# Kernel optimization log

Hardware: AMD Instinct MI355X
Metric: run time of the kernel (lower is better)

Reference implementation:

```python
import jax, jax.numpy as jnp
import numpy as np

PF_DIM = 1024
F_DIM = 1024
LOW = 128
MID = 32  # low_dim // 4
BATCH = 8192


def setup_inputs() -> dict:
    key = jax.random.key(0)
    ks = jax.random.split(key, 10)
    s = lambda fan_in: 1.0 / np.sqrt(fan_in)
    return {
        "f": jax.random.normal(ks[0], (BATCH, F_DIM), jnp.float32),
        "pf": jax.random.normal(ks[1], (BATCH, PF_DIM), jnp.float32),
        # nn.Linear weights are (out, in)
        "proj_f_w": jax.random.uniform(ks[2], (LOW, F_DIM), jnp.float32, -s(F_DIM), s(F_DIM)),
        "proj_f_b": jax.random.uniform(ks[3], (LOW,), jnp.float32, -s(F_DIM), s(F_DIM)),
        "proj_pf_w": jax.random.uniform(ks[4], (LOW, PF_DIM), jnp.float32, -s(PF_DIM), s(PF_DIM)),
        "proj_pf_b": jax.random.uniform(ks[5], (LOW,), jnp.float32, -s(PF_DIM), s(PF_DIM)),
        "proj_f2_w": jax.random.uniform(ks[6], (F_DIM, LOW), jnp.float32, -s(LOW), s(LOW)),
        "proj_f2_b": jax.random.uniform(ks[7], (F_DIM,), jnp.float32, -s(LOW), s(LOW)),
        "pg_w": jax.random.uniform(ks[8], (2 * LOW * MID, LOW), jnp.float32, -s(LOW), s(LOW)),
        "pg_b": jax.random.uniform(ks[9], (2 * LOW * MID,), jnp.float32, -s(LOW), s(LOW)),
    }


def reference(f, pf, proj_f_w, proj_f_b, proj_pf_w, proj_pf_b,
              proj_f2_w, proj_f2_b, pg_w, pg_b):
    b = pf.shape[0]
    # project both inputs to low_dim
    f_low = f @ proj_f_w.T + proj_f_b              # (b, LOW)
    pf_low = pf @ proj_pf_w.T + proj_pf_b          # (b, LOW)
    # per-sample generated weights
    params = pf_low @ pg_w.T + pg_b                # (b, 2*LOW*MID)
    dim = LOW * MID
    p1 = params[:, :dim].reshape(b, LOW, MID)      # (b, LOW, MID)
    p2 = params[:, dim:].reshape(b, MID, LOW)      # (b, MID, LOW)
    # batched tiny MLP: (b,1,LOW)@(b,LOW,MID) -> relu -> @(b,MID,LOW)
    h = jax.nn.relu(jnp.einsum('bl,blm->bm', f_low, p1))
    g = jnp.einsum('bm,bml->bl', h, p2)            # (b, LOW)
    out = g @ proj_f2_w.T + proj_f2_b + f + pf     # (b, F_DIM)
    return out
```

## Files before the change

### kernel.cpp

```cpp
#include <hip/hip_runtime.h>
#include <hip/hip_bf16.h>
#include <stdint.h>


typedef __attribute__((ext_vector_type(8))) short bf16x8;
typedef __attribute__((ext_vector_type(4))) float f32x4;

#define MFMA(a, b, c) __builtin_amdgcn_mfma_f32_16x16x32_bf16((a), (b), (c), 0, 0, 0)

__device__ __forceinline__ ushort f2bf(float x) {
    union { float f; uint32_t u; } v; v.f = x;
    return (ushort)((v.u + 0x7FFFu + ((v.u >> 16) & 1u)) >> 16);
}
__device__ __forceinline__ ushort4 f2bf4(float4 v) {
    ushort4 o; o.x = f2bf(v.x); o.y = f2bf(v.y); o.z = f2bf(v.z); o.w = f2bf(v.w); return o;
}

__global__ __launch_bounds__(256) void k0_convert(
    const float* __restrict__ pgw, const float* __restrict__ wf,
    const float* __restrict__ wpf, const float* __restrict__ w2,
    ushort* __restrict__ pg_img, ushort* __restrict__ w_img, ushort* __restrict__ w2_img)
{
    int cid = blockIdx.x * 256 + threadIdx.x;
    const float* src; ushort* dst;
    if (cid < 131072) {
        int lane = cid & 63, ks = (cid >> 6) & 3, T = cid >> 8;
        int j = T * 16 + (lane & 15), k = ks * 32 + (lane >> 4) * 8;
        src = pgw + (size_t)j * 128 + k;
        dst = pg_img + (size_t)cid * 8;
    } else if (cid < 163840) {
        int c = cid - 131072;
        int lane = c & 63, ks = (c >> 6) & 31, lt = (c >> 11) & 7, mat = c >> 14;
        int l = lt * 16 + (lane & 15), k = ks * 32 + (lane >> 4) * 8;
        src = (mat ? wpf : wf) + (size_t)l * 1024 + k;
        dst = w_img + (size_t)c * 8;
    } else {
        int c = cid - 163840;
        int lane = c & 63, ks = (c >> 6) & 3, nt = c >> 8;
        int n = nt * 16 + (lane & 15), k = ks * 32 + (lane >> 4) * 8;
        src = w2 + (size_t)n * 128 + k;
        dst = w2_img + (size_t)c * 8;
    }
    float4 a = ((const float4*)src)[0], b = ((const float4*)src)[1];
    ((ushort4*)dst)[0] = f2bf4(a);
    ((ushort4*)dst)[1] = f2bf4(b);
}

__global__ __launch_bounds__(256, 4) void k1_proj(
    const float* __restrict__ f, const float* __restrict__ pf,
    const ushort* __restrict__ w_img,
    const float* __restrict__ bf_bias, const float* __restrict__ bpf_bias,
    float* __restrict__ f_low , ushort* __restrict__ pf_img )
{
    __shared__ __align__(16) ushort As[16 * 1032];
    __shared__ __align__(16) ushort Tr[16 * 136];
    const int tid = threadIdx.x;
    const int lane = tid & 63, wid = tid >> 6;
    const int q = lane >> 4, r15 = lane & 15;
    const int mat = blockIdx.x & 1;
    const int b0 = (blockIdx.x >> 1) * 16;
    const float* src = mat ? pf : f;
    const float* bias_ptr = mat ? bpf_bias : bf_bias;

#pragma unroll
    for (int ch = 0; ch < 2; ch++) {
        float4 v[8];
#pragma unroll
        for (int rr = 0; rr < 8; rr++)
            v[rr] = *(const float4*)(src + (size_t)(b0 + ch * 8 + rr) * 1024 + tid * 4);
#pragma unroll
        for (int rr = 0; rr < 8; rr++)
            *(ushort4*)(As + (ch * 8 + rr) * 1032 + tid * 4) = f2bf4(v[rr]);
    }
    float bias_v[2];
#pragma unroll
    for (int j = 0; j < 2; j++) bias_v[j] = bias_ptr[wid * 32 + j * 16 + r15];
    __syncthreads();

    const int lt0 = wid * 2;
    const ushort* wb = w_img + (size_t)mat * 131072;
    bf16x8 wfr[4][2];
#pragma unroll
    for (int pre = 0; pre < 4; pre++)
#pragma unroll
        for (int j = 0; j < 2; j++)
            wfr[pre][j] = *(const bf16x8*)(wb + ((size_t)(lt0 + j) * 32 + pre) * 512 + lane * 8);

    f32x4 c[2];
    c[0] = (f32x4){0.f, 0.f, 0.f, 0.f};
    c[1] = (f32x4){0.f, 0.f, 0.f, 0.f};
#pragma unroll
    for (int ks = 0; ks < 32; ks++) {
        const int cur = ks & 3;
        bf16x8 af = *(const bf16x8*)(As + r15 * 1032 + ks * 32 + q * 8);
        c[0] = MFMA(af, wfr[cur][0], c[0]);
        c[1] = MFMA(af, wfr[cur][1], c[1]);
        if (ks + 4 < 32) {
#pragma unroll
            for (int j = 0; j < 2; j++)
                wfr[cur][j] = *(const bf16x8*)(wb + ((size_t)(lt0 + j) * 32 + (ks + 4)) * 512 + lane * 8);
        }
    }
    if (mat == 0) {
#pragma unroll
        for (int j = 0; j < 2; j++) {
            int l = wid * 32 + j * 16 + r15;
#pragma unroll
            for (int r = 0; r < 4; r++)
                f_low[(size_t)l * 8192 + b0 + q * 4 + r] = c[j][r] + bias_v[j];
        }
    } else {
#pragma unroll
        for (int j = 0; j < 2; j++) {
            int l = wid * 32 + j * 16 + r15;
#pragma unroll
            for (int r = 0; r < 4; r++)
                Tr[(q * 4 + r) * 136 + l] = f2bf(c[j][r] + bias_v[j]);
        }
        __syncthreads();
        int ks2 = tid >> 6, ln = tid & 63;
        int b_loc = ln & 15, k0 = ks2 * 32 + (ln >> 4) * 8;
        uint4 tv = *(const uint4*)(Tr + b_loc * 136 + k0);
        *(uint4*)(pf_img + ((size_t)((b0 >> 4) * 4 + ks2)) * 512 + (size_t)ln * 8) = tv;
    }
}

__global__ __launch_bounds__(256, 4) void k2_h(
    const ushort* __restrict__ pg_img, const ushort* __restrict__ pf_img,
    const float* __restrict__ pg_b, const float* __restrict__ f_low,
    float* __restrict__ h_part )
{
    __shared__ __align__(16) float flow[16 * 32];
    __shared__ __align__(16) float biasl[512];
    __shared__ __align__(16) float hred[4 * 32 * 32];
    const int tid = threadIdx.x;
    const int lane = tid & 63, wid = tid >> 6;
    const int q = lane >> 4, r15 = lane & 15;
    const int jg = blockIdx.x & 7, sb = blockIdx.x >> 3;
    const int b0 = sb * 32;

    bf16x8 bfr[2][4];
#pragma unroll
    for (int ct = 0; ct < 2; ct++)
#pragma unroll
        for (int ks = 0; ks < 4; ks++)
            bfr[ct][ks] = *(const bf16x8*)(pf_img + ((size_t)((sb * 2 + ct) * 4 + ks)) * 512 + lane * 8);

    if (tid < 128) {
        int row = tid >> 3, c4 = (tid & 7) * 4;
        *(float4*)(flow + row * 32 + c4) =
            *(const float4*)(f_low + (size_t)(jg * 16 + row) * 8192 + b0 + c4);
    } else {
        int t = tid - 128;
        *(float4*)(biasl + t * 4) = *(const float4*)(pg_b + jg * 512 + t * 4);
    }
    __syncthreads();

    f32x4 hacc[2][2];
#pragma unroll
    for (int i = 0; i < 2; i++)
#pragma unroll
        for (int j = 0; j < 2; j++) hacc[i][j] = (f32x4){0.f, 0.f, 0.f, 0.f};

    const ushort* Tbase = pg_img + (size_t)(jg * 32 + wid * 8) * 2048;
    bf16x8 af[2][4];
#pragma unroll
    for (int ks = 0; ks < 4; ks++) af[0][ks] = *(const bf16x8*)(Tbase + ks * 512 + lane * 8);
#pragma unroll
    for (int i = 0; i < 8; i++) {
        const int cur = i & 1, nxt = cur ^ 1;
        if (i < 7) {
#pragma unroll
            for (int ks = 0; ks < 4; ks++)
                af[nxt][ks] = *(const bf16x8*)(Tbase + (size_t)(i + 1) * 2048 + ks * 512 + lane * 8);
        }
        const int tl = wid * 8 + i;
        const int l_loc = tl >> 1, mh = tl & 1;
        f32x4 bv = *(const f32x4*)(biasl + tl * 16 + q * 4);
#pragma unroll
        for (int ct = 0; ct < 2; ct++) {
            f32x4 cc = (f32x4){0.f, 0.f, 0.f, 0.f};
#pragma unroll
            for (int ks = 0; ks < 4; ks++) cc = MFMA(af[cur][ks], bfr[ct][ks], cc);
            float s = flow[l_loc * 32 + ct * 16 + r15];
#pragma unroll
            for (int r = 0; r < 4; r++) hacc[mh][ct][r] += s * (cc[r] + bv[r]);
        }
    }
#pragma unroll
    for (int mh = 0; mh < 2; mh++)
#pragma unroll
        for (int ct = 0; ct < 2; ct++)
#pragma unroll
            for (int r = 0; r < 4; r++)
                hred[wid * 1024 + (mh * 16 + q * 4 + r) * 32 + ct * 16 + r15] = hacc[mh][ct][r];
    __syncthreads();
    {
        int m = tid >> 3, bq = (tid & 7) * 4;
        const float* h0 = hred + m * 32 + bq;
        float4 s;
        s.x = h0[0] + h0[1024] + h0[2048] + h0[3072];
        s.y = h0[1] + h0[1025] + h0[2049] + h0[3073];
        s.z = h0[2] + h0[1026] + h0[2050] + h0[3074];
        s.w = h0[3] + h0[1027] + h0[2051] + h0[3075];
        *(float4*)(h_part + (size_t)jg * 262144 + (size_t)m * 8192 + b0 + bq) = s;
    }
}

__global__ __launch_bounds__(256, 4) void k2_g(
    const ushort* __restrict__ pg_img, const ushort* __restrict__ pf_img,
    const float* __restrict__ pg_b, const float* __restrict__ h_part,
    ushort* __restrict__ g_img )
{
    __shared__ __align__(16) float hl[32 * 32];
    __shared__ __align__(16) float biasl[32 * 32];
    __shared__ __align__(16) float gred[4 * 32 * 32];
    const int tid = threadIdx.x;
    const int lane = tid & 63, wid = tid >> 6;
    const int q = lane >> 4, r15 = lane & 15;
    const int lg = blockIdx.x & 3, sb = blockIdx.x >> 2;
    const int b0 = sb * 32;

    bf16x8 bfr[2][4];
#pragma unroll
    for (int ct = 0; ct < 2; ct++)
#pragma unroll
        for (int ks = 0; ks < 4; ks++)
            bfr[ct][ks] = *(const bf16x8*)(pf_img + ((size_t)((sb * 2 + ct) * 4 + ks)) * 512 + lane * 8);

    {
        int m = tid >> 3, c4 = (tid & 7) * 4;
        float4 s = (float4){0.f, 0.f, 0.f, 0.f};
#pragma unroll
        for (int g = 0; g < 8; g++) {
            float4 a = *(const float4*)(h_part + (size_t)g * 262144 + (size_t)m * 8192 + b0 + c4);
            s.x += a.x; s.y += a.y; s.z += a.z; s.w += a.w;
        }
        s.x = fmaxf(s.x, 0.f); s.y = fmaxf(s.y, 0.f); s.z = fmaxf(s.z, 0.f); s.w = fmaxf(s.w, 0.f);
        *(float4*)(hl + m * 32 + c4) = s;
        *(float4*)(biasl + m * 32 + c4) =
            *(const float4*)(pg_b + 4096 + (size_t)m * 128 + lg * 32 + c4);
    }
    __syncthreads();

    f32x4 gacc[2][2];
#pragma unroll
    for (int i = 0; i < 2; i++)
#pragma unroll
        for (int j = 0; j < 2; j++) gacc[i][j] = (f32x4){0.f, 0.f, 0.f, 0.f};

    bf16x8 af[2][4];
#pragma unroll
    for (int ks = 0; ks < 4; ks++)
        af[0][ks] = *(const bf16x8*)(pg_img + (size_t)(256 + wid * 8 + lg * 2) * 2048 + ks * 512 + lane * 8);
#pragma unroll
    for (int ti = 0; ti < 16; ti++) {
        const int cur = ti & 1, nxt = cur ^ 1;
        if (ti < 15) {
            const int tn = ti + 1;
            const int mn = wid + 4 * (tn >> 1), ltn = tn & 1;
            const ushort* ap = pg_img + (size_t)(256 + mn * 8 + lg * 2 + ltn) * 2048;
#pragma unroll
            for (int ks = 0; ks < 4; ks++)
                af[nxt][ks] = *(const bf16x8*)(ap + ks * 512 + lane * 8);
        }
        const int m = wid + 4 * (ti >> 1), lt = ti & 1;
        f32x4 bv = *(const f32x4*)(biasl + m * 32 + lt * 16 + q * 4);
#pragma unroll
        for (int ct = 0; ct < 2; ct++) {
            f32x4 cc = (f32x4){0.f, 0.f, 0.f, 0.f};
#pragma unroll
            for (int ks = 0; ks < 4; ks++) cc = MFMA(af[cur][ks], bfr[ct][ks], cc);
            float s = hl[m * 32 + ct * 16 + r15];
#pragma unroll
            for (int r = 0; r < 4; r++) gacc[lt][ct][r] += s * (cc[r] + bv[r]);
        }
    }
#pragma unroll
    for (int lt = 0; lt < 2; lt++)
#pragma unroll
        for (int ct = 0; ct < 2; ct++)
#pragma unroll
            for (int r = 0; r < 4; r++)
                gred[wid * 1024 + (lt * 16 + q * 4 + r) * 32 + ct * 16 + r15] = gacc[lt][ct][r];
    __syncthreads();
    if (tid < 128) {
        int bt = tid >> 6, ln = tid & 63;
        int b_loc = bt * 16 + (ln & 15);
        int l0 = (ln >> 4) * 8;
        ushort tmp[8];
#pragma unroll
        for (int e = 0; e < 8; e++) {
            const float* gp = gred + (l0 + e) * 32 + b_loc;
            tmp[e] = f2bf(gp[0] + gp[1024] + gp[2048] + gp[3072]);
        }
        ushort4 lo = {tmp[0], tmp[1], tmp[2], tmp[3]};
        ushort4 hi = {tmp[4], tmp[5], tmp[6], tmp[7]};
        ushort* dst = g_img + ((size_t)((sb * 2 + bt) * 4 + lg)) * 512 + (size_t)ln * 8;
        ((ushort4*)dst)[0] = lo;
        ((ushort4*)dst)[1] = hi;
    }
}

__global__ __launch_bounds__(256, 4) void k3_out(
    const ushort* __restrict__ g_img, const ushort* __restrict__ w2_img,
    const float* __restrict__ b2, const float* __restrict__ f,
    const float* __restrict__ pf, float* __restrict__ out)
{
    __shared__ __align__(16) float Ls[32 * 288];
    const int tid = threadIdx.x;
    const int lane = tid & 63, wid = tid >> 6;
    const int q = lane >> 4, r15 = lane & 15;
    const int sb = blockIdx.x >> 2, nb = blockIdx.x & 3;
    const int b0 = sb * 32, n0 = nb * 256;

    float bias_v[4];
#pragma unroll
    for (int nt = 0; nt < 4; nt++) bias_v[nt] = b2[n0 + wid * 64 + nt * 16 + r15];

    bf16x8 af[2][4];
#pragma unroll
    for (int mtl = 0; mtl < 2; mtl++)
#pragma unroll
        for (int ks = 0; ks < 4; ks++)
            af[mtl][ks] = *(const bf16x8*)(g_img + ((size_t)((sb * 2 + mtl) * 4 + ks)) * 512 + lane * 8);
    bf16x8 wfr[2][4];
#pragma unroll
    for (int ks = 0; ks < 4; ks++)
        wfr[0][ks] = *(const bf16x8*)(w2_img + ((size_t)((nb * 16 + wid * 4) * 4 + ks)) * 512 + lane * 8);
#pragma unroll
    for (int nt = 0; nt < 4; nt++) {
        const int cur = nt & 1, nxt = cur ^ 1;
        if (nt < 3) {
#pragma unroll
            for (int ks = 0; ks < 4; ks++)
                wfr[nxt][ks] = *(const bf16x8*)(w2_img + ((size_t)((nb * 16 + wid * 4 + nt + 1) * 4 + ks)) * 512 + lane * 8);
        }
#pragma unroll
        for (int mtl = 0; mtl < 2; mtl++) {
            f32x4 cc = (f32x4){0.f, 0.f, 0.f, 0.f};
#pragma unroll
            for (int ks = 0; ks < 4; ks++) cc = MFMA(af[mtl][ks], wfr[cur][ks], cc);
            const int nloc = wid * 64 + nt * 16 + r15;
            const int chunk = nloc >> 5, within = nloc & 31;
#pragma unroll
            for (int r = 0; r < 4; r++)
                Ls[(mtl * 16 + q * 4 + r) * 288 + chunk * 36 + within] = cc[r] + bias_v[nt];
        }
    }
    __syncthreads();
    {
        const float* ls = Ls + (wid * 8) * 288 + (lane >> 3) * 36 + (lane & 7) * 4;
#pragma unroll
        for (int rr = 0; rr < 8; rr++) {
            const int b = b0 + wid * 8 + rr;
            const size_t gbase = (size_t)b * 1024 + n0 + lane * 4;
            float4 lv = *(const float4*)(ls + rr * 288);
            float4 fa = *(const float4*)(f + gbase);
            float4 pa = *(const float4*)(pf + gbase);
            float4 o;
            o.x = lv.x + fa.x + pa.x; o.y = lv.y + fa.y + pa.y;
            o.z = lv.z + fa.z + pa.z; o.w = lv.w + fa.w + pa.w;
            *(float4*)(out + gbase) = o;
        }
    }
}

extern "C" void kernel_launch(void* const* d_in, const int* in_sizes, int n_in,
                              void* d_out, int out_size, void* d_ws, size_t ws_size,
                              hipStream_t stream)
{
    const float* f    = (const float*)d_in[0];
    const float* pf   = (const float*)d_in[1];
    const float* wf   = (const float*)d_in[2];
    const float* bfb  = (const float*)d_in[3];
    const float* wpf  = (const float*)d_in[4];
    const float* bpfb = (const float*)d_in[5];
    const float* w2   = (const float*)d_in[6];
    const float* b2   = (const float*)d_in[7];
    const float* pgw  = (const float*)d_in[8];
    const float* pgb  = (const float*)d_in[9];

    char* ws = (char*)d_ws;
    ushort* pg_img = (ushort*)(ws + 0);
    ushort* w_img  = (ushort*)(ws + 2097152);
    ushort* w2_img = (ushort*)(ws + 2621440);
    float*  f_low  = (float*)(ws + 2883584);
    ushort* pf_img = (ushort*)(ws + 7077888);
    float*  h_part = (float*)(ws + 9175040);
    ushort* g_img  = (ushort*)(ws + 17563648);
    float*  out    = (float*)d_out;

    k0_convert<<<dim3(704), dim3(256), 0, stream>>>(pgw, wf, wpf, w2, pg_img, w_img, w2_img);
    k1_proj<<<dim3(1024), dim3(256), 0, stream>>>(f, pf, w_img, bfb, bpfb, f_low, pf_img);
    k2_h<<<dim3(2048), dim3(256), 0, stream>>>(pg_img, pf_img, pgb, f_low, h_part);
    k2_g<<<dim3(1024), dim3(256), 0, stream>>>(pg_img, pf_img, pgb, h_part, g_img);
    k3_out<<<dim3(1024), dim3(256), 0, stream>>>(g_img, w2_img, b2, f, pf, out);
}
```

Before: 183.1 us.

## Fuse projection, generated-MLP, and output kernels into one persistent mega kernel

Merges the four compute kernels into a single kernel where each block owns 32 batch rows and runs the projections, the h and g stages, and the output GEMM plus residual add, keeping intermediates in shared memory. This removes the global round trips for f_low, pf_img, h_part and g_img, and cuts three kernel launches. The cost is only 256 blocks at one block per CU, with serialized loops inside each block. That leaves little latency hiding and makes each block re-stream the whole generated-weight image from L2.

```diff
diff --git a/kernel.cpp b/kernel.cpp
--- a/kernel.cpp
+++ b/kernel.cpp
@@ -1,5 +1,4 @@
 #include <hip/hip_runtime.h>
-#include <hip/hip_bf16.h>
 #include <stdint.h>
 
 
@@ -14,6 +13,9 @@
 }
 __device__ __forceinline__ ushort4 f2bf4(float4 v) {
     ushort4 o; o.x = f2bf(v.x); o.y = f2bf(v.y); o.z = f2bf(v.z); o.w = f2bf(v.w); return o;
+}
+__device__ __forceinline__ float bf2f(ushort u) {
+    union { uint32_t i; float f; } v; v.i = ((uint32_t)u) << 16; return v.f;
 }
 
 __global__ __launch_bounds__(256) void k0_convert(
@@ -46,145 +48,143 @@
     ((ushort4*)dst)[1] = f2bf4(b);
 }
 
-__global__ __launch_bounds__(256, 4) void k1_proj(
+__global__ __launch_bounds__(256, 1) void mega(
     const float* __restrict__ f, const float* __restrict__ pf,
-    const ushort* __restrict__ w_img,
-    const float* __restrict__ bf_bias, const float* __restrict__ bpf_bias,
-    float* __restrict__ f_low , ushort* __restrict__ pf_img )
+    const ushort* __restrict__ w_img, const float* __restrict__ bfb,
+    const float* __restrict__ bpfb, const ushort* __restrict__ pg_img,
+    const float* __restrict__ pgb, const ushort* __restrict__ w2_img,
+    const float* __restrict__ b2, float* __restrict__ out)
 {
-    __shared__ __align__(16) ushort As[16 * 1032];
-    __shared__ __align__(16) ushort Tr[16 * 136];
+    __shared__ __align__(16) char smem[62464];
+    ushort* As    = (ushort*)smem;
+    ushort* Tr    = (ushort*)smem;
+    float*  hred  = (float*)smem;
+    float*  hl    = (float*)(smem + 16384);
+    float*  gred  = (float*)smem;
+    float*  Ls    = (float*)smem;
+    ushort* flowT = (ushort*)(smem + 36864);
+    ushort* pfrag = (ushort*)(smem + 46080);
+    ushort* gfrag = (ushort*)(smem + 54272);
+
     const int tid = threadIdx.x;
     const int lane = tid & 63, wid = tid >> 6;
     const int q = lane >> 4, r15 = lane & 15;
-    const int mat = blockIdx.x & 1;
-    const int b0 = (blockIdx.x >> 1) * 16;
-    const float* src = mat ? pf : f;
-    const float* bias_ptr = mat ? bpf_bias : bf_bias;
-
-#pragma unroll
-    for (int ch = 0; ch < 2; ch++) {
-        float4 v[8];
-#pragma unroll
-        for (int rr = 0; rr < 8; rr++)
-            v[rr] = *(const float4*)(src + (size_t)(b0 + ch * 8 + rr) * 1024 + tid * 4);
-#pragma unroll
-        for (int rr = 0; rr < 8; rr++)
-            *(ushort4*)(As + (ch * 8 + rr) * 1032 + tid * 4) = f2bf4(v[rr]);
-    }
-    float bias_v[2];
-#pragma unroll
-    for (int j = 0; j < 2; j++) bias_v[j] = bias_ptr[wid * 32 + j * 16 + r15];
+    const int b0 = blockIdx.x * 32;
+
+#pragma unroll 1
+    for (int mat = 0; mat < 2; mat++) {
+        const float* src = mat ? pf : f;
+        const float* bias_ptr = mat ? bpfb : bfb;
+        float bias_v[2];
+#pragma unroll
+        for (int j = 0; j < 2; j++) bias_v[j] = bias_ptr[wid * 32 + j * 16 + r15];
+
+        f32x4 c[2][2];
+        c[0][0] = c[0][1] = c[1][0] = c[1][1] = (f32x4){0.f, 0.f, 0.f, 0.f};
+
+#pragma unroll 1
+        for (int kh = 0; kh < 2; kh++) {
+            __syncthreads();
+#pragma unroll
+            for (int half = 0; half < 2; half++) {
+                float4 v[8];
+#pragma unroll
+                for (int rr = 0; rr < 8; rr++) {
+                    int row = (half * 8 + rr) * 2 + (tid >> 7);
+                    v[rr] = *(const float4*)(src + (size_t)(b0 + row) * 1024 + kh * 512 + (tid & 127) * 4);
+                }
+#pragma unroll
+                for (int rr = 0; rr < 8; rr++) {
+                    int row = (half * 8 + rr) * 2 + (tid >> 7);
+                    *(ushort4*)(As + row * 520 + (tid & 127) * 4) = f2bf4(v[rr]);
+                }
+            }
+            __syncthreads();
+            const int lt0 = wid * 2;
+#pragma unroll
+            for (int ks = 0; ks < 16; ks++) {
+                bf16x8 w0 = *(const bf16x8*)(w_img + (size_t)mat * 131072 + ((size_t)(lt0 + 0) * 32 + kh * 16 + ks) * 512 + lane * 8);
+                bf16x8 w1 = *(const bf16x8*)(w_img + (size_t)mat * 131072 + ((size_t)(lt0 + 1) * 32 + kh * 16 + ks) * 512 + lane * 8);
+                bf16x8 a0 = *(const bf16x8*)(As + (0 * 16 + r15) * 520 + ks * 32 + q * 8);
+                bf16x8 a1 = *(const bf16x8*)(As + (1 * 16 + r15) * 520 + ks * 32 + q * 8);
+                c[0][0] = MFMA(a0, w0, c[0][0]);
+                c[0][1] = MFMA(a0, w1, c[0][1]);
+                c[1][0] = MFMA(a1, w0, c[1][0]);
+                c[1][1] = MFMA(a1, w1, c[1][1]);
+            }
+        }
+        if (mat == 0) {
+#pragma unroll
+            for (int mt = 0; mt < 2; mt++)
+#pragma unroll
+                for (int j = 0; j < 2; j++) {
+                    int l = wid * 32 + j * 16 + r15;
+#pragma unroll
+                    for (int r = 0; r < 4; r++)
+                        flowT[l * 36 + mt * 16 + q * 4 + r] = f2bf(c[mt][j][r] + bias_v[j]);
+                }
+        } else {
+            __syncthreads();
+#pragma unroll
+            for (int mt = 0; mt < 2; mt++)
+#pragma unroll
+                for (int j = 0; j < 2; j++) {
+                    int l = wid * 32 + j * 16 + r15;
+#pragma unroll
+                    for (int r = 0; r < 4; r++)
+                        Tr[(mt * 16 + q * 4 + r) * 136 + l] = f2bf(c[mt][j][r] + bias_v[j]);
+                }
+            __syncthreads();
+#pragma unroll
+            for (int pass = 0; pass < 2; pass++) {
+                int chunkid = pass * 4 + (tid >> 6);
+                int bt = chunkid >> 2, ks2 = chunkid & 3;
+                int ln = tid & 63;
+                int k0 = ks2 * 32 + (ln >> 4) * 8;
+                uint4 tv = *(const uint4*)(Tr + (bt * 16 + (ln & 15)) * 136 + k0);
+                *(uint4*)(pfrag + (size_t)chunkid * 512 + ln * 8) = tv;
+            }
+        }
+    }
     __syncthreads();
 
-    const int lt0 = wid * 2;
-    const ushort* wb = w_img + (size_t)mat * 131072;
-    bf16x8 wfr[4][2];
-#pragma unroll
-    for (int pre = 0; pre < 4; pre++)
-#pragma unroll
-        for (int j = 0; j < 2; j++)
-            wfr[pre][j] = *(const bf16x8*)(wb + ((size_t)(lt0 + j) * 32 + pre) * 512 + lane * 8);
-
-    f32x4 c[2];
-    c[0] = (f32x4){0.f, 0.f, 0.f, 0.f};
-    c[1] = (f32x4){0.f, 0.f, 0.f, 0.f};
-#pragma unroll
-    for (int ks = 0; ks < 32; ks++) {
-        const int cur = ks & 3;
-        bf16x8 af = *(const bf16x8*)(As + r15 * 1032 + ks * 32 + q * 8);
-        c[0] = MFMA(af, wfr[cur][0], c[0]);
-        c[1] = MFMA(af, wfr[cur][1], c[1]);
-        if (ks + 4 < 32) {
-#pragma unroll
-            for (int j = 0; j < 2; j++)
-                wfr[cur][j] = *(const bf16x8*)(wb + ((size_t)(lt0 + j) * 32 + (ks + 4)) * 512 + lane * 8);
-        }
-    }
-    if (mat == 0) {
-#pragma unroll
-        for (int j = 0; j < 2; j++) {
-            int l = wid * 32 + j * 16 + r15;
-#pragma unroll
-            for (int r = 0; r < 4; r++)
-                f_low[(size_t)l * 8192 + b0 + q * 4 + r] = c[j][r] + bias_v[j];
-        }
-    } else {
-#pragma unroll
-        for (int j = 0; j < 2; j++) {
-            int l = wid * 32 + j * 16 + r15;
-#pragma unroll
-            for (int r = 0; r < 4; r++)
-                Tr[(q * 4 + r) * 136 + l] = f2bf(c[j][r] + bias_v[j]);
-        }
-        __syncthreads();
-        int ks2 = tid >> 6, ln = tid & 63;
-        int b_loc = ln & 15, k0 = ks2 * 32 + (ln >> 4) * 8;
-        uint4 tv = *(const uint4*)(Tr + b_loc * 136 + k0);
-        *(uint4*)(pf_img + ((size_t)((b0 >> 4) * 4 + ks2)) * 512 + (size_t)ln * 8) = tv;
-    }
-}
-
-__global__ __launch_bounds__(256, 4) void k2_h(
-    const ushort* __restrict__ pg_img, const ushort* __restrict__ pf_img,
-    const float* __restrict__ pg_b, const float* __restrict__ f_low,
-    float* __restrict__ h_part )
-{
-    __shared__ __align__(16) float flow[16 * 32];
-    __shared__ __align__(16) float biasl[512];
-    __shared__ __align__(16) float hred[4 * 32 * 32];
-    const int tid = threadIdx.x;
-    const int lane = tid & 63, wid = tid >> 6;
-    const int q = lane >> 4, r15 = lane & 15;
-    const int jg = blockIdx.x & 7, sb = blockIdx.x >> 3;
-    const int b0 = sb * 32;
-
     bf16x8 bfr[2][4];
 #pragma unroll
     for (int ct = 0; ct < 2; ct++)
 #pragma unroll
         for (int ks = 0; ks < 4; ks++)
-            bfr[ct][ks] = *(const bf16x8*)(pf_img + ((size_t)((sb * 2 + ct) * 4 + ks)) * 512 + lane * 8);
-
-    if (tid < 128) {
-        int row = tid >> 3, c4 = (tid & 7) * 4;
-        *(float4*)(flow + row * 32 + c4) =
-            *(const float4*)(f_low + (size_t)(jg * 16 + row) * 8192 + b0 + c4);
-    } else {
-        int t = tid - 128;
-        *(float4*)(biasl + t * 4) = *(const float4*)(pg_b + jg * 512 + t * 4);
-    }
-    __syncthreads();
+            bfr[ct][ks] = *(const bf16x8*)(pfrag + (size_t)(ct * 4 + ks) * 512 + lane * 8);
 
     f32x4 hacc[2][2];
-#pragma unroll
-    for (int i = 0; i < 2; i++)
-#pragma unroll
-        for (int j = 0; j < 2; j++) hacc[i][j] = (f32x4){0.f, 0.f, 0.f, 0.f};
-
-    const ushort* Tbase = pg_img + (size_t)(jg * 32 + wid * 8) * 2048;
-    bf16x8 af[2][4];
-#pragma unroll
-    for (int ks = 0; ks < 4; ks++) af[0][ks] = *(const bf16x8*)(Tbase + ks * 512 + lane * 8);
-#pragma unroll
-    for (int i = 0; i < 8; i++) {
-        const int cur = i & 1, nxt = cur ^ 1;
-        if (i < 7) {
-#pragma unroll
-            for (int ks = 0; ks < 4; ks++)
-                af[nxt][ks] = *(const bf16x8*)(Tbase + (size_t)(i + 1) * 2048 + ks * 512 + lane * 8);
-        }
-        const int tl = wid * 8 + i;
-        const int l_loc = tl >> 1, mh = tl & 1;
-        f32x4 bv = *(const f32x4*)(biasl + tl * 16 + q * 4);
-#pragma unroll
-        for (int ct = 0; ct < 2; ct++) {
-            f32x4 cc = (f32x4){0.f, 0.f, 0.f, 0.f};
-#pragma unroll
-            for (int ks = 0; ks < 4; ks++) cc = MFMA(af[cur][ks], bfr[ct][ks], cc);
-            float s = flow[l_loc * 32 + ct * 16 + r15];
-#pragma unroll
-            for (int r = 0; r < 4; r++) hacc[mh][ct][r] += s * (cc[r] + bv[r]);
+    hacc[0][0] = hacc[0][1] = hacc[1][0] = hacc[1][1] = (f32x4){0.f, 0.f, 0.f, 0.f};
+
+#pragma unroll 1
+    for (int jg = 0; jg < 8; jg++) {
+        const ushort* Tbase = pg_img + (size_t)(jg * 32 + wid * 8) * 2048;
+        bf16x8 af[2][4];
+#pragma unroll
+        for (int ks = 0; ks < 4; ks++) af[0][ks] = *(const bf16x8*)(Tbase + ks * 512 + lane * 8);
+#pragma unroll
+        for (int i = 0; i < 8; i++) {
+            const int cur = i & 1, nxt = cur ^ 1;
+            if (i < 7) {
+#pragma unroll
+                for (int ks = 0; ks < 4; ks++)
+                    af[nxt][ks] = *(const bf16x8*)(Tbase + (size_t)(i + 1) * 2048 + ks * 512 + lane * 8);
+            }
+            const int tl = wid * 8 + i;
+            const int mh = tl & 1;
+            f32x4 bv = *(const f32x4*)(pgb + (size_t)(jg * 32 + tl) * 16 + q * 4);
+            const int fbase = (jg * 16 + (tl >> 1)) * 36;
+#pragma unroll
+            for (int ct = 0; ct < 2; ct++) {
+                f32x4 cc = (f32x4){0.f, 0.f, 0.f, 0.f};
+#pragma unroll
+                for (int ks = 0; ks < 4; ks++) cc = MFMA(af[cur][ks], bfr[ct][ks], cc);
+                float s = bf2f(flowT[fbase + ct * 16 + r15]);
+#pragma unroll
+                for (int r = 0; r < 4; r++) hacc[mh][ct][r] += s * (cc[r] + bv[r]);
+            }
         }
     }
 #pragma unroll
@@ -199,170 +199,126 @@
         int m = tid >> 3, bq = (tid & 7) * 4;
         const float* h0 = hred + m * 32 + bq;
         float4 s;
-        s.x = h0[0] + h0[1024] + h0[2048] + h0[3072];
-        s.y = h0[1] + h0[1025] + h0[2049] + h0[3073];
-        s.z = h0[2] + h0[1026] + h0[2050] + h0[3074];
-        s.w = h0[3] + h0[1027] + h0[2051] + h0[3075];
-        *(float4*)(h_part + (size_t)jg * 262144 + (size_t)m * 8192 + b0 + bq) = s;
-    }
-}
-
-__global__ __launch_bounds__(256, 4) void k2_g(
-    const ushort* __restrict__ pg_img, const ushort* __restrict__ pf_img,
-    const float* __restrict__ pg_b, const float* __restrict__ h_part,
-    ushort* __restrict__ g_img )
-{
-    __shared__ __align__(16) float hl[32 * 32];
-    __shared__ __align__(16) float biasl[32 * 32];
-    __shared__ __align__(16) float gred[4 * 32 * 32];
-    const int tid = threadIdx.x;
-    const int lane = tid & 63, wid = tid >> 6;
-    const int q = lane >> 4, r15 = lane & 15;
-    const int lg = blockIdx.x & 3, sb = blockIdx.x >> 2;
-    const int b0 = sb * 32;
-
-    bf16x8 bfr[2][4];
-#pragma unroll
-    for (int ct = 0; ct < 2; ct++)
+        s.x = fmaxf(h0[0] + h0[1024] + h0[2048] + h0[3072], 0.f);
+        s.y = fmaxf(h0[1] + h0[1025] + h0[2049] + h0[3073], 0.f);
+        s.z = fmaxf(h0[2] + h0[1026] + h0[2050] + h0[3074], 0.f);
+        s.w = fmaxf(h0[3] + h0[1027] + h0[2051] + h0[3075], 0.f);
+        *(float4*)(hl + m * 32 + bq) = s;
+    }
+    __syncthreads();
+
+#pragma unroll 1
+    for (int lg = 0; lg < 4; lg++) {
+        f32x4 gacc[2][2];
+        gacc[0][0] = gacc[0][1] = gacc[1][0] = gacc[1][1] = (f32x4){0.f, 0.f, 0.f, 0.f};
+        bf16x8 af[2][4];
 #pragma unroll
         for (int ks = 0; ks < 4; ks++)
-            bfr[ct][ks] = *(const bf16x8*)(pf_img + ((size_t)((sb * 2 + ct) * 4 + ks)) * 512 + lane * 8);
-
-    {
-        int m = tid >> 3, c4 = (tid & 7) * 4;
-        float4 s = (float4){0.f, 0.f, 0.f, 0.f};
-#pragma unroll
-        for (int g = 0; g < 8; g++) {
-            float4 a = *(const float4*)(h_part + (size_t)g * 262144 + (size_t)m * 8192 + b0 + c4);
-            s.x += a.x; s.y += a.y; s.z += a.z; s.w += a.w;
-        }
-        s.x = fmaxf(s.x, 0.f); s.y = fmaxf(s.y, 0.f); s.z = fmaxf(s.z, 0.f); s.w = fmaxf(s.w, 0.f);
-        *(float4*)(hl + m * 32 + c4) = s;
-        *(float4*)(biasl + m * 32 + c4) =
-            *(const float4*)(pg_b + 4096 + (size_t)m * 128 + lg * 32 + c4);
-    }
-    __syncthreads();
-
-    f32x4 gacc[2][2];
-#pragma unroll
-    for (int i = 0; i < 2; i++)
-#pragma unroll
-        for (int j = 0; j < 2; j++) gacc[i][j] = (f32x4){0.f, 0.f, 0.f, 0.f};
-
-    bf16x8 af[2][4];
-#pragma unroll
-    for (int ks = 0; ks < 4; ks++)
-        af[0][ks] = *(const bf16x8*)(pg_img + (size_t)(256 + wid * 8 + lg * 2) * 2048 + ks * 512 + lane * 8);
-#pragma unroll
-    for (int ti = 0; ti < 16; ti++) {
-        const int cur = ti & 1, nxt = cur ^ 1;
-        if (ti < 15) {
-            const int tn = ti + 1;
-            const int mn = wid + 4 * (tn >> 1), ltn = tn & 1;
-            const ushort* ap = pg_img + (size_t)(256 + mn * 8 + lg * 2 + ltn) * 2048;
-#pragma unroll
-            for (int ks = 0; ks < 4; ks++)
-                af[nxt][ks] = *(const bf16x8*)(ap + ks * 512 + lane * 8);
-        }
-        const int m = wid + 4 * (ti >> 1), lt = ti & 1;
-        f32x4 bv = *(const f32x4*)(biasl + m * 32 + lt * 16 + q * 4);
-#pragma unroll
-        for (int ct = 0; ct < 2; ct++) {
-            f32x4 cc = (f32x4){0.f, 0.f, 0.f, 0.f};
-#pragma unroll
-            for (int ks = 0; ks < 4; ks++) cc = MFMA(af[cur][ks], bfr[ct][ks], cc);
-            float s = hl[m * 32 + ct * 16 + r15];
-#pragma unroll
-            for (int r = 0; r < 4; r++) gacc[lt][ct][r] += s * (cc[r] + bv[r]);
-        }
-    }
-#pragma unroll
-    for (int lt = 0; lt < 2; lt++)
-#pragma unroll
-        for (int ct = 0; ct < 2; ct++)
-#pragma unroll
-            for (int r = 0; r < 4; r++)
-                gred[wid * 1024 + (lt * 16 + q * 4 + r) * 32 + ct * 16 + r15] = gacc[lt][ct][r];
-    __syncthreads();
-    if (tid < 128) {
-        int bt = tid >> 6, ln = tid & 63;
-        int b_loc = bt * 16 + (ln & 15);
-        int l0 = (ln >> 4) * 8;
-        ushort tmp[8];
-#pragma unroll
-        for (int e = 0; e < 8; e++) {
-            const float* gp = gred + (l0 + e) * 32 + b_loc;
-            tmp[e] = f2bf(gp[0] + gp[1024] + gp[2048] + gp[3072]);
-        }
-        ushort4 lo = {tmp[0], tmp[1], tmp[2], tmp[3]};
-        ushort4 hi = {tmp[4], tmp[5], tmp[6], tmp[7]};
-        ushort* dst = g_img + ((size_t)((sb * 2 + bt) * 4 + lg)) * 512 + (size_t)ln * 8;
-        ((ushort4*)dst)[0] = lo;
-        ((ushort4*)dst)[1] = hi;
-    }
-}
-
-__global__ __launch_bounds__(256, 4) void k3_out(
-    const ushort* __restrict__ g_img, const ushort* __restrict__ w2_img,
-    const float* __restrict__ b2, const float* __restrict__ f,
-    const float* __restrict__ pf, float* __restrict__ out)
-{
-    __shared__ __align__(16) float Ls[32 * 288];
-    const int tid = threadIdx.x;
-    const int lane = tid & 63, wid = tid >> 6;
-    const int q = lane >> 4, r15 = lane & 15;
-    const int sb = blockIdx.x >> 2, nb = blockIdx.x & 3;
-    const int b0 = sb * 32, n0 = nb * 256;
-
-    float bias_v[4];
-#pragma unroll
-    for (int nt = 0; nt < 4; nt++) bias_v[nt] = b2[n0 + wid * 64 + nt * 16 + r15];
-
-    bf16x8 af[2][4];
+            af[0][ks] = *(const bf16x8*)(pg_img + (size_t)(256 + wid * 8 + lg * 2) * 2048 + ks * 512 + lane * 8);
+#pragma unroll
+        for (int ti = 0; ti < 16; ti++) {
+            const int cur = ti & 1, nxt = cur ^ 1;
+            if (ti < 15) {
+                const int tn = ti + 1;
+                const int mn = wid + 4 * (tn >> 1), ltn = tn & 1;
+                const ushort* ap = pg_img + (size_t)(256 + mn * 8 + lg * 2 + ltn) * 2048;
+#pragma unroll
+                for (int ks = 0; ks < 4; ks++)
+                    af[nxt][ks] = *(const bf16x8*)(ap + ks * 512 + lane * 8);
+            }
+            const int m = wid + 4 * (ti >> 1), lt = ti & 1;
+            f32x4 bv = *(const f32x4*)(pgb + 4096 + (size_t)m * 128 + lg * 32 + lt * 16 + q * 4);
+#pragma unroll
+            for (int ct = 0; ct < 2; ct++) {
+                f32x4 cc = (f32x4){0.f, 0.f, 0.f, 0.f};
+#pragma unroll
+                for (int ks = 0; ks < 4; ks++) cc = MFMA(af[cur][ks], bfr[ct][ks], cc);
+                float s = hl[m * 32 + ct * 16 + r15];
+#pragma unroll
+                for (int r = 0; r < 4; r++) gacc[lt][ct][r] += s * (cc[r] + bv[r]);
+            }
+        }
+#pragma unroll
+        for (int lt = 0; lt < 2; lt++)
+#pragma unroll
+            for (int ct = 0; ct < 2; ct++)
+#pragma unroll
+                for (int r = 0; r < 4; r++)
+                    gred[wid * 1024 + (lt * 16 + q * 4 + r) * 32 + ct * 16 + r15] = gacc[lt][ct][r];
+        __syncthreads();
+        if (tid < 128) {
+            int bt = tid >> 6, ln = tid & 63;
+            int b_loc = bt * 16 + (ln & 15);
+            int l0 = (ln >> 4) * 8;
+            ushort tmp[8];
+#pragma unroll
+            for (int e = 0; e < 8; e++) {
+                const float* gp = gred + (l0 + e) * 32 + b_loc;
+                tmp[e] = f2bf(gp[0] + gp[1024] + gp[2048] + gp[3072]);
+            }
+            ushort4 lo = {tmp[0], tmp[1], tmp[2], tmp[3]};
+            ushort4 hi = {tmp[4], tmp[5], tmp[6], tmp[7]};
+            ushort* dst = gfrag + (size_t)(bt * 4 + lg) * 512 + ln * 8;
+            ((ushort4*)dst)[0] = lo;
+            ((ushort4*)dst)[1] = hi;
+        }
+        __syncthreads();
+    }
+
+    bf16x8 afg[2][4];
 #pragma unroll
     for (int mtl = 0; mtl < 2; mtl++)
 #pragma unroll
         for (int ks = 0; ks < 4; ks++)
-            af[mtl][ks] = *(const bf16x8*)(g_img + ((size_t)((sb * 2 + mtl) * 4 + ks)) * 512 + lane * 8);
-    bf16x8 wfr[2][4];
-#pragma unroll
-    for (int ks = 0; ks < 4; ks++)
-        wfr[0][ks] = *(const bf16x8*)(w2_img + ((size_t)((nb * 16 + wid * 4) * 4 + ks)) * 512 + lane * 8);
-#pragma unroll
-    for (int nt = 0; nt < 4; nt++) {
-        const int cur = nt & 1, nxt = cur ^ 1;
-        if (nt < 3) {
-#pragma unroll
-            for (int ks = 0; ks < 4; ks++)
-                wfr[nxt][ks] = *(const bf16x8*)(w2_img + ((size_t)((nb * 16 + wid * 4 + nt + 1) * 4 + ks)) * 512 + lane * 8);
-        }
-#pragma unroll
-        for (int mtl = 0; mtl < 2; mtl++) {
-            f32x4 cc = (f32x4){0.f, 0.f, 0.f, 0.f};
-#pragma unroll
-            for (int ks = 0; ks < 4; ks++) cc = MFMA(af[mtl][ks], wfr[cur][ks], cc);
-            const int nloc = wid * 64 + nt * 16 + r15;
-            const int chunk = nloc >> 5, within = nloc & 31;
-#pragma unroll
-            for (int r = 0; r < 4; r++)
-                Ls[(mtl * 16 + q * 4 + r) * 288 + chunk * 36 + within] = cc[r] + bias_v[nt];
-        }
-    }
-    __syncthreads();
-    {
-        const float* ls = Ls + (wid * 8) * 288 + (lane >> 3) * 36 + (lane & 7) * 4;
-#pragma unroll
-        for (int rr = 0; rr < 8; rr++) {
-            const int b = b0 + wid * 8 + rr;
-            const size_t gbase = (size_t)b * 1024 + n0 + lane * 4;
-            float4 lv = *(const float4*)(ls + rr * 288);
-            float4 fa = *(const float4*)(f + gbase);
-            float4 pa = *(const float4*)(pf + gbase);
-            float4 o;
-            o.x = lv.x + fa.x + pa.x; o.y = lv.y + fa.y + pa.y;
-            o.z = lv.z + fa.z + pa.z; o.w = lv.w + fa.w + pa.w;
-            *(float4*)(out + gbase) = o;
-        }
+            afg[mtl][ks] = *(const bf16x8*)(gfrag + (size_t)(mtl * 4 + ks) * 512 + lane * 8);
+
+#pragma unroll 1
+    for (int nb = 0; nb < 4; nb++) {
+        float bias_v4[4];
+#pragma unroll
+        for (int nt = 0; nt < 4; nt++) bias_v4[nt] = b2[nb * 256 + wid * 64 + nt * 16 + r15];
+        bf16x8 wfr[2][4];
+#pragma unroll
+        for (int ks = 0; ks < 4; ks++)
+            wfr[0][ks] = *(const bf16x8*)(w2_img + (size_t)((nb * 16 + wid * 4) * 4 + ks) * 512 + lane * 8);
+#pragma unroll
+        for (int nt = 0; nt < 4; nt++) {
+            const int cur = nt & 1, nxt = cur ^ 1;
+            if (nt < 3) {
+#pragma unroll
+                for (int ks = 0; ks < 4; ks++)
+                    wfr[nxt][ks] = *(const bf16x8*)(w2_img + (size_t)((nb * 16 + wid * 4 + nt + 1) * 4 + ks) * 512 + lane * 8);
+            }
+#pragma unroll
+            for (int mtl = 0; mtl < 2; mtl++) {
+                f32x4 cc = (f32x4){0.f, 0.f, 0.f, 0.f};
+#pragma unroll
+                for (int ks = 0; ks < 4; ks++) cc = MFMA(afg[mtl][ks], wfr[cur][ks], cc);
+                const int nloc = wid * 64 + nt * 16 + r15;
+                const int chunk = nloc >> 5, within = nloc & 31;
+#pragma unroll
+                for (int r = 0; r < 4; r++)
+                    Ls[(mtl * 16 + q * 4 + r) * 288 + chunk * 36 + within] = cc[r] + bias_v4[nt];
+            }
+        }
+        __syncthreads();
+        {
+            const float* ls = Ls + (wid * 8) * 288 + (lane >> 3) * 36 + (lane & 7) * 4;
+            const int n0 = nb * 256;
+#pragma unroll
+            for (int rr = 0; rr < 8; rr++) {
+                const int b = b0 + wid * 8 + rr;
+                const size_t gbase = (size_t)b * 1024 + n0 + lane * 4;
+                float4 lv = *(const float4*)(ls + rr * 288);
+                float4 fa = *(const float4*)(f + gbase);
+                float4 pa = *(const float4*)(pf + gbase);
+                float4 o;
+                o.x = lv.x + fa.x + pa.x; o.y = lv.y + fa.y + pa.y;
+                o.z = lv.z + fa.z + pa.z; o.w = lv.w + fa.w + pa.w;
+                *(float4*)(out + gbase) = o;
+            }
+        }
+        __syncthreads();
     }
 }
 
@@ -385,15 +341,9 @@
     ushort* pg_img = (ushort*)(ws + 0);
     ushort* w_img  = (ushort*)(ws + 2097152);
     ushort* w2_img = (ushort*)(ws + 2621440);
-    float*  f_low  = (float*)(ws + 2883584);
-    ushort* pf_img = (ushort*)(ws + 7077888);
-    float*  h_part = (float*)(ws + 9175040);
-    ushort* g_img  = (ushort*)(ws + 17563648);
     float*  out    = (float*)d_out;
 
     k0_convert<<<dim3(704), dim3(256), 0, stream>>>(pgw, wf, wpf, w2, pg_img, w_img, w2_img);
-    k1_proj<<<dim3(1024), dim3(256), 0, stream>>>(f, pf, w_img, bfb, bpfb, f_low, pf_img);
-    k2_h<<<dim3(2048), dim3(256), 0, stream>>>(pg_img, pf_img, pgb, f_low, h_part);
-    k2_g<<<dim3(1024), dim3(256), 0, stream>>>(pg_img, pf_img, pgb, h_part, g_img);
-    k3_out<<<dim3(1024), dim3(256), 0, stream>>>(g_img, w2_img, b2, f, pf, out);
-}
+    mega<<<dim3(256), dim3(256), 0, stream>>>(f, pf, w_img, bfb, bpfb,
+                                              pg_img, pgb, w2_img, b2, out);
+}
```

Measured after the change: 192.1 us. 1.05x slower.
